# Performance work log

Measured on AMD Instinct MI355X. Metric: run time of the kernel, lower is better.

The kernel has to match this reference:

```python
import jax, jax.numpy as jnp
import numpy as np

B, C, H, W = 32, 64, 64, 64
NUM_CODES = 1024
COMMITMENT_COST = 0.25


def setup_inputs() -> dict:
    key = jax.random.key(0)
    k1, k2 = jax.random.split(key)
    z = jax.random.normal(k1, (B, C, H, W), dtype=jnp.float32)
    # matches nn.Embedding init uniform_(-1/num_codes, 1/num_codes)
    codebook = jax.random.uniform(k2, (NUM_CODES, C), dtype=jnp.float32,
                                  minval=-1.0 / NUM_CODES, maxval=1.0 / NUM_CODES)
    return {"z": z, "codebook": codebook}


def reference(z, codebook):
    # b c h w -> b h w c
    zt = jnp.transpose(z, (0, 2, 3, 1))
    b, h, w, c = zt.shape
    z_flat = zt.reshape(-1, c)  # (N, c)

    # squared L2 distances to each code: ||z||^2 + ||e||^2 - 2 z.e
    d = (jnp.sum(z_flat * z_flat, axis=1, keepdims=True)
         + jnp.sum(codebook * codebook, axis=1)[None, :]
         - 2.0 * z_flat @ codebook.T)  # (N, K)
    indices = jnp.argmin(d, axis=1)  # (N,)

    z_q = codebook[indices].reshape(b, h, w, c)

    codebook_loss = jnp.mean((z_q - jax.lax.stop_gradient(zt)) ** 2)
    commitment_loss = jnp.mean((zt - jax.lax.stop_gradient(z_q)) ** 2)
    loss = codebook_loss + COMMITMENT_COST * commitment_loss

    # straight-through estimator
    z_q_st = zt + jax.lax.stop_gradient(z_q - zt)
    z_q_out = jnp.transpose(z_q_st, (0, 3, 1, 2))  # b h w c -> b c h w
    return z_q_out, loss, indices.reshape(b, h, w)
```

## Files before the change

### kernel.cpp

```cpp
#include <hip/hip_runtime.h>

#define CDIM 64
#define KCODES 1024
#define ZQ_ELEMS (32 * 64 * 64 * 64)
#define NROWS 131072
#define FLT_BIG 3.402823466e38f
#define RPB 64
#define NBLK (NROWS / RPB)
#define CSTRIDE 49
#define DELTA 5e-4f

#define WS_BSQ_OFF 16384
#define WS_E1_OFF  32768

#define SK_RD_OFF 12544
#define SK_RK_OFF (12544 + 1024)
#define SU_BYTES  (12544 + 2048)

typedef __bf16 bf16x8 __attribute__((ext_vector_type(8)));
typedef float  f32x4  __attribute__((ext_vector_type(4)));

__device__ __forceinline__ float pairwise_sq64(const float* v) {
    float r[8];
    #pragma unroll
    for (int j = 0; j < 8; ++j) r[j] = __fmul_rn(v[j], v[j]);
    #pragma unroll
    for (int m = 1; m < 8; ++m) {
        #pragma unroll
        for (int j = 0; j < 8; ++j)
            r[j] = __fadd_rn(r[j], __fmul_rn(v[8 * m + j], v[8 * m + j]));
    }
    return __fadd_rn(__fadd_rn(__fadd_rn(r[0], r[1]), __fadd_rn(r[2], r[3])),
                     __fadd_rn(__fadd_rn(r[4], r[5]), __fadd_rn(r[6], r[7])));
}

__global__ __launch_bounds__(256) void vq_prep(const float* __restrict__ cb,
                                               float* __restrict__ Bsq,
                                               __bf16* __restrict__ e1) {
    const int k = blockIdx.x * 256 + threadIdx.x;
    const float* __restrict__ ck = cb + k * CDIM;
    float v[CDIM];
    #pragma unroll
    for (int q = 0; q < 16; ++q) {
        float4 t = ((const float4*)ck)[q];
        v[4 * q + 0] = t.x; v[4 * q + 1] = t.y; v[4 * q + 2] = t.z; v[4 * q + 3] = t.w;
    }
    Bsq[k] = pairwise_sq64(v);

    const int t = k >> 4, kin = k & 15;
    bf16x8* F1 = (bf16x8*)e1;
    #pragma unroll
    for (int ks = 0; ks < 2; ++ks) {
        #pragma unroll
        for (int g = 0; g < 4; ++g) {
            bf16x8 a;
            #pragma unroll
            for (int i = 0; i < 8; ++i) a[i] = (__bf16)v[ks * 32 + 8 * g + i];
            F1[(t * 2 + ks) * 64 + ((g << 4) | kin)] = a;
        }
    }
}

#define INS(j, accv, Bv, code0) \
    { \
        const float vv = __fmaf_rn(-2.f, (accv), (Bv)); \
        const float kk = __int_as_float((__float_as_int(vv) & 0xFFFFFC00) | (code0)); \
        const float o0 = K0[j], o1 = K1[j], o2 = K2[j]; \
        K0[j] = fminf(o0, kk); \
        K1[j] = __builtin_amdgcn_fmed3f(o0, o1, kk); \
        K2[j] = __builtin_amdgcn_fmed3f(o1, o2, kk); \
    }

#define TILE_COMPUTE(Ea, Eb, code0) \
    { \
        const float Bv = sB[code0]; \
        f32x4 a0 = __builtin_amdgcn_mfma_f32_16x16x32_bf16(zA0, Ea, zero, 0, 0, 0); \
        a0       = __builtin_amdgcn_mfma_f32_16x16x32_bf16(zA1, Eb, a0, 0, 0, 0); \
        INS(0, a0[0], Bv, code0) INS(1, a0[1], Bv, code0) \
        INS(2, a0[2], Bv, code0) INS(3, a0[3], Bv, code0) \
    }

__global__ __launch_bounds__(256, 4) void vq_main(const float* __restrict__ z,
                                                  const float* __restrict__ cb,
                                                  const float* __restrict__ Bsq,
                                                  const __bf16* __restrict__ e1,
                                                  float* __restrict__ zq_out,
                                                  float* __restrict__ idx_out,
                                                  double* __restrict__ part) {
    __shared__ __align__(16) unsigned char sU[SU_BYTES];
    __shared__ float sB[KCODES];

    const int tid = threadIdx.x;
    const int n0 = blockIdx.x * RPB;
    const int b = n0 >> 12;
    const int hw0 = n0 & 4095;
    const float* __restrict__ zb = z + ((size_t)b << 18) + hw0;

    for (int k = tid; k < KCODES; k += 256) sB[k] = Bsq[k];

    {
        bf16x8* __restrict__ zfw = (bf16x8*)sU;
        const int r = tid & 63;
        const int hh = tid >> 6;
        const int H = hh >> 1, G = hh & 1;
        const int w = r >> 4, li = r & 15;
        #pragma unroll
        for (int gg = 0; gg < 2; ++gg) {
            const int g = G * 2 + gg;
            bf16x8 hi;
            #pragma unroll
            for (int i = 0; i < 8; ++i) {
                const float fv = zb[((size_t)(32 * H + 8 * g + i) << 12) + r];
                hi[i] = (__bf16)fv;
            }
            zfw[(w * 2 + H) * 65 + ((g << 4) | li)] = hi;
        }
    }
    __syncthreads();

    const int lane = tid & 63, w = tid >> 6;
    const int g = lane >> 4, li = lane & 15;

    const bf16x8* __restrict__ zf = (const bf16x8*)sU;
    const bf16x8 zA0 = zf[(w * 2 + 0) * 65 + lane];
    const bf16x8 zA1 = zf[(w * 2 + 1) * 65 + lane];

    float K0[4], K1[4], K2[4];
    #pragma unroll
    for (int j = 0; j < 4; ++j) { K0[j] = FLT_BIG; K1[j] = FLT_BIG; K2[j] = FLT_BIG; }

    const bf16x8* __restrict__ pe1 = (const bf16x8*)e1 + lane;
    const f32x4 zero = {0.f, 0.f, 0.f, 0.f};

    bf16x8 A1a = pe1[0], A1b = pe1[64];
    int tb = li;

    for (int t = 0; t < 64; t += 2) {
        const int o1 = (t + 1) * 128;
        const int o2 = (t + 2) * 128;
        bf16x8 B1a = pe1[o1], B1b = pe1[o1 + 64];
        TILE_COMPUTE(A1a, A1b, tb)
        A1a = pe1[o2]; A1b = pe1[o2 + 64];
        TILE_COMPUTE(B1a, B1b, tb + 16)
        tb += 32;
    }

    __syncthreads();

    float* __restrict__ sKey = (float*)sU;
    float* __restrict__ sRd = (float*)(sU + SK_RD_OFF);
    int*   __restrict__ sRk = (int*)(sU + SK_RK_OFF);
    #pragma unroll
    for (int j = 0; j < 4; ++j) {
        const int row = 16 * w + 4 * g + j;
        const int base = row * CSTRIDE + li * 3;
        sKey[base + 0] = K0[j];
        sKey[base + 1] = K1[j];
        sKey[base + 2] = K2[j];
    }
    __syncthreads();

    const int r = tid & 63;
    const int quarter = tid >> 6;
    const int n = n0 + r;

    float gmin = FLT_BIG;
    #pragma unroll
    for (int s2 = 0; s2 < 48; ++s2) gmin = fminf(gmin, sKey[r * CSTRIDE + s2]);
    const float thr = gmin + DELTA;

    float zrow[CDIM];
    const float* __restrict__ zp = zb + r;
    #pragma unroll
    for (int c = 0; c < CDIM; ++c) zrow[c] = zp[(size_t)c << 12];
    const float A = pairwise_sq64(zrow);

    float bd = FLT_BIG;
    int bk = 1 << 30;
    const int sbeg = quarter * 12;
    for (int s2 = sbeg; s2 < sbeg + 12; ++s2) {
        const float kv = sKey[r * CSTRIDE + s2];
        if (kv <= thr) {
            const int k = __float_as_int(kv) & 0x3FF;
            const float4* __restrict__ ek = (const float4*)(cb + (size_t)k * CDIM);
            float m = 0.f;
            #pragma unroll
            for (int q = 0; q < 16; ++q) {
                float4 e = ek[q];
                m = __fmaf_rn(zrow[4 * q + 0], e.x, m);
                m = __fmaf_rn(zrow[4 * q + 1], e.y, m);
                m = __fmaf_rn(zrow[4 * q + 2], e.z, m);
                m = __fmaf_rn(zrow[4 * q + 3], e.w, m);
            }
            const float d = __fsub_rn(__fadd_rn(A, sB[k]), __fadd_rn(m, m));
            if (d < bd || (d == bd && k < bk)) { bd = d; bk = k; }
        }
    }

    sRd[tid] = bd;
    sRk[tid] = bk;
    __syncthreads();

    if (tid < RPB) {
        #pragma unroll
        for (int qq = 1; qq < 4; ++qq) {
            const float d2 = sRd[qq * 64 + r];
            const int   k2 = sRk[qq * 64 + r];
            if (d2 < bd || (d2 == bd && k2 < bk)) { bd = d2; bk = k2; }
        }

        idx_out[n] = (float)bk;

        const float4* __restrict__ cq = (const float4*)(cb + (size_t)bk * CDIM);
        float* __restrict__ zo = zq_out + ((size_t)b << 18) + hw0 + r;
        float lsum = 0.f;
        #pragma unroll
        for (int q = 0; q < 16; ++q) {
            float4 qv = cq[q];
            zo[(size_t)(4 * q + 0) << 12] = qv.x;
            zo[(size_t)(4 * q + 1) << 12] = qv.y;
            zo[(size_t)(4 * q + 2) << 12] = qv.z;
            zo[(size_t)(4 * q + 3) << 12] = qv.w;
            lsum = fmaf(qv.x - zrow[4 * q + 0], qv.x - zrow[4 * q + 0], lsum);
            lsum = fmaf(qv.y - zrow[4 * q + 1], qv.y - zrow[4 * q + 1], lsum);
            lsum = fmaf(qv.z - zrow[4 * q + 2], qv.z - zrow[4 * q + 2], lsum);
            lsum = fmaf(qv.w - zrow[4 * q + 3], qv.w - zrow[4 * q + 3], lsum);
        }

        double ls = (double)lsum;
        for (int off = 32; off > 0; off >>= 1) ls += __shfl_down(ls, off, 64);
        if (tid == 0) part[blockIdx.x] = ls;
    }
}

__global__ void vq_finalize(const double* __restrict__ part, float* __restrict__ loss_out) {
    __shared__ double s[16];
    const int tid = threadIdx.x;
    double v = part[tid] + part[tid + 1024];
    for (int off = 32; off > 0; off >>= 1) v += __shfl_down(v, off, 64);
    if ((tid & 63) == 0) s[tid >> 6] = v;
    __syncthreads();
    if (tid == 0) {
        double t = 0.0;
        #pragma unroll
        for (int i = 0; i < 16; ++i) t += s[i];
        *loss_out = (float)(1.25 * t / (double)ZQ_ELEMS);
    }
}

extern "C" void kernel_launch(void* const* d_in, const int* in_sizes, int n_in,
                              void* d_out, int out_size, void* d_ws, size_t ws_size,
                              hipStream_t stream) {
    const float* z  = (const float*)d_in[0];
    const float* cb = (const float*)d_in[1];
    float* out  = (float*)d_out;
    float* zq   = out;
    float* loss = out + ZQ_ELEMS;
    float* idx  = out + ZQ_ELEMS + 1;
    char* ws = (char*)d_ws;
    double* part = (double*)ws;
    float* Bsq   = (float*)(ws + WS_BSQ_OFF);
    __bf16* e1   = (__bf16*)(ws + WS_E1_OFF);

    vq_prep<<<4, 256, 0, stream>>>(cb, Bsq, e1);
    vq_main<<<NBLK, 256, 0, stream>>>(z, cb, Bsq, e1, zq, idx, part);
    vq_finalize<<<1, 1024, 0, stream>>>(part, loss);
}
```

Measured before the change: 75.90 us.

## Share codebook fragments across waves via double-buffered LDS with bigger blocks

Each block now handles 128 rows with 512 threads instead of 64 rows with 256. The bf16 codebook fragments are staged through a double-buffered LDS tile that all eight waves share, rather than each wave streaming them from global memory on its own. This cuts global/L2 traffic for the codebook and halves the number of per-block partial sums. The cost is a block-wide barrier on every codebook chunk, and launch bounds of (512, 4) tighten the register budget, which risks spilling the 64-float zrow array. The prefetch on the last iteration also reads past the end of the e1 buffer.

```diff
diff --git a/kernel.cpp b/kernel.cpp
--- a/kernel.cpp
+++ b/kernel.cpp
@@ -5,17 +5,22 @@
 #define ZQ_ELEMS (32 * 64 * 64 * 64)
 #define NROWS 131072
 #define FLT_BIG 3.402823466e38f
-#define RPB 64
+#define RPB 128
 #define NBLK (NROWS / RPB)
+#define NTHR 512
 #define CSTRIDE 49
 #define DELTA 5e-4f
 
 #define WS_BSQ_OFF 16384
 #define WS_E1_OFF  32768
 
-#define SK_RD_OFF 12544
-#define SK_RK_OFF (12544 + 1024)
-#define SU_BYTES  (12544 + 2048)
+#define B_OFF     0
+#define FRAG_OFF  4096
+#define E_OFF     20736
+#define SKEY_OFF  4096
+#define SK_RD_OFF 29184
+#define SK_RK_OFF 31232
+#define SU_BYTES  33280
 
 typedef __bf16 bf16x8 __attribute__((ext_vector_type(8)));
 typedef float  f32x4  __attribute__((ext_vector_type(4)));
@@ -80,7 +85,7 @@
         INS(2, a0[2], Bv, code0) INS(3, a0[3], Bv, code0) \
     }
 
-__global__ __launch_bounds__(256, 4) void vq_main(const float* __restrict__ z,
+__global__ __launch_bounds__(512, 4) void vq_main(const float* __restrict__ z,
                                                   const float* __restrict__ cb,
                                                   const float* __restrict__ Bsq,
                                                   const __bf16* __restrict__ e1,
@@ -88,7 +93,8 @@
                                                   float* __restrict__ idx_out,
                                                   double* __restrict__ part) {
     __shared__ __align__(16) unsigned char sU[SU_BYTES];
-    __shared__ float sB[KCODES];
+    __shared__ double sP2[2];
+    float* __restrict__ sB = (float*)(sU + B_OFF);
 
     const int tid = threadIdx.x;
     const int n0 = blockIdx.x * RPB;
@@ -96,13 +102,13 @@
     const int hw0 = n0 & 4095;
     const float* __restrict__ zb = z + ((size_t)b << 18) + hw0;
 
-    for (int k = tid; k < KCODES; k += 256) sB[k] = Bsq[k];
+    for (int k = tid; k < KCODES; k += NTHR) sB[k] = Bsq[k];
 
     {
-        bf16x8* __restrict__ zfw = (bf16x8*)sU;
-        const int r = tid & 63;
-        const int hh = tid >> 6;
-        const int H = hh >> 1, G = hh & 1;
+        bf16x8* __restrict__ zfw = (bf16x8*)(sU + FRAG_OFF);
+        const int r = tid & 127;
+        const int q4 = tid >> 7;
+        const int H = q4 >> 1, G = q4 & 1;
         const int w = r >> 4, li = r & 15;
         #pragma unroll
         for (int gg = 0; gg < 2; ++gg) {
@@ -115,13 +121,15 @@
             }
             zfw[(w * 2 + H) * 65 + ((g << 4) | li)] = hi;
         }
+        *(float2*)(sU + E_OFF + tid * 8) =
+            *(const float2*)((const unsigned char*)e1 + tid * 8);
     }
     __syncthreads();
 
     const int lane = tid & 63, w = tid >> 6;
     const int g = lane >> 4, li = lane & 15;
 
-    const bf16x8* __restrict__ zf = (const bf16x8*)sU;
+    const bf16x8* __restrict__ zf = (const bf16x8*)(sU + FRAG_OFF);
     const bf16x8 zA0 = zf[(w * 2 + 0) * 65 + lane];
     const bf16x8 zA1 = zf[(w * 2 + 1) * 65 + lane];
 
@@ -129,25 +137,20 @@
     #pragma unroll
     for (int j = 0; j < 4; ++j) { K0[j] = FLT_BIG; K1[j] = FLT_BIG; K2[j] = FLT_BIG; }
 
-    const bf16x8* __restrict__ pe1 = (const bf16x8*)e1 + lane;
     const f32x4 zero = {0.f, 0.f, 0.f, 0.f};
 
-    bf16x8 A1a = pe1[0], A1b = pe1[64];
-    int tb = li;
-
-    for (int t = 0; t < 64; t += 2) {
-        const int o1 = (t + 1) * 128;
-        const int o2 = (t + 2) * 128;
-        bf16x8 B1a = pe1[o1], B1b = pe1[o1 + 64];
-        TILE_COMPUTE(A1a, A1b, tb)
-        A1a = pe1[o2]; A1b = pe1[o2 + 64];
-        TILE_COMPUTE(B1a, B1b, tb + 16)
-        tb += 32;
-    }
-
-    __syncthreads();
-
-    float* __restrict__ sKey = (float*)sU;
+    for (int c = 0; c < 32; ++c) {
+        const float2 vstage =
+            *(const float2*)((const unsigned char*)e1 + (c + 1) * 4096 + tid * 8);
+        const bf16x8* __restrict__ buf = (const bf16x8*)(sU + E_OFF + (c & 1) * 4096);
+        const int cb0 = c * 32 + li;
+        TILE_COMPUTE(buf[lane],       buf[64 + lane],  cb0)
+        *(float2*)(sU + E_OFF + ((c + 1) & 1) * 4096 + tid * 8) = vstage;
+        TILE_COMPUTE(buf[128 + lane], buf[192 + lane], cb0 + 16)
+        __syncthreads();
+    }
+
+    float* __restrict__ sKey = (float*)(sU + SKEY_OFF);
     float* __restrict__ sRd = (float*)(sU + SK_RD_OFF);
     int*   __restrict__ sRk = (int*)(sU + SK_RK_OFF);
     #pragma unroll
@@ -160,83 +163,87 @@
     }
     __syncthreads();
 
-    const int r = tid & 63;
-    const int quarter = tid >> 6;
-    const int n = n0 + r;
-
-    float gmin = FLT_BIG;
-    #pragma unroll
-    for (int s2 = 0; s2 < 48; ++s2) gmin = fminf(gmin, sKey[r * CSTRIDE + s2]);
-    const float thr = gmin + DELTA;
-
-    float zrow[CDIM];
-    const float* __restrict__ zp = zb + r;
-    #pragma unroll
-    for (int c = 0; c < CDIM; ++c) zrow[c] = zp[(size_t)c << 12];
-    const float A = pairwise_sq64(zrow);
-
-    float bd = FLT_BIG;
-    int bk = 1 << 30;
-    const int sbeg = quarter * 12;
-    for (int s2 = sbeg; s2 < sbeg + 12; ++s2) {
-        const float kv = sKey[r * CSTRIDE + s2];
-        if (kv <= thr) {
-            const int k = __float_as_int(kv) & 0x3FF;
-            const float4* __restrict__ ek = (const float4*)(cb + (size_t)k * CDIM);
-            float m = 0.f;
+    {
+        const int r = tid & 127;
+        const int quarter = tid >> 7;
+        const int n = n0 + r;
+
+        float gmin = FLT_BIG;
+        #pragma unroll
+        for (int s2 = 0; s2 < 48; ++s2) gmin = fminf(gmin, sKey[r * CSTRIDE + s2]);
+        const float thr = gmin + DELTA;
+
+        float zrow[CDIM];
+        const float* __restrict__ zp = zb + r;
+        #pragma unroll
+        for (int c = 0; c < CDIM; ++c) zrow[c] = zp[(size_t)c << 12];
+        const float A = pairwise_sq64(zrow);
+
+        float bd = FLT_BIG;
+        int bk = 1 << 30;
+        const int sbeg = quarter * 12;
+        for (int s2 = sbeg; s2 < sbeg + 12; ++s2) {
+            const float kv = sKey[r * CSTRIDE + s2];
+            if (kv <= thr) {
+                const int k = __float_as_int(kv) & 0x3FF;
+                const float4* __restrict__ ek = (const float4*)(cb + (size_t)k * CDIM);
+                float m = 0.f;
+                #pragma unroll
+                for (int q = 0; q < 16; ++q) {
+                    float4 e = ek[q];
+                    m = __fmaf_rn(zrow[4 * q + 0], e.x, m);
+                    m = __fmaf_rn(zrow[4 * q + 1], e.y, m);
+                    m = __fmaf_rn(zrow[4 * q + 2], e.z, m);
+                    m = __fmaf_rn(zrow[4 * q + 3], e.w, m);
+                }
+                const float d = __fsub_rn(__fadd_rn(A, sB[k]), __fadd_rn(m, m));
+                if (d < bd || (d == bd && k < bk)) { bd = d; bk = k; }
+            }
+        }
+
+        sRd[tid] = bd;
+        sRk[tid] = bk;
+        __syncthreads();
+
+        if (tid < RPB) {
+            #pragma unroll
+            for (int qq = 1; qq < 4; ++qq) {
+                const float d2 = sRd[qq * 128 + r];
+                const int   k2 = sRk[qq * 128 + r];
+                if (d2 < bd || (d2 == bd && k2 < bk)) { bd = d2; bk = k2; }
+            }
+
+            idx_out[n] = (float)bk;
+
+            const float4* __restrict__ cq = (const float4*)(cb + (size_t)bk * CDIM);
+            float* __restrict__ zo = zq_out + ((size_t)b << 18) + hw0 + r;
+            float lsum = 0.f;
             #pragma unroll
             for (int q = 0; q < 16; ++q) {
-                float4 e = ek[q];
-                m = __fmaf_rn(zrow[4 * q + 0], e.x, m);
-                m = __fmaf_rn(zrow[4 * q + 1], e.y, m);
-                m = __fmaf_rn(zrow[4 * q + 2], e.z, m);
-                m = __fmaf_rn(zrow[4 * q + 3], e.w, m);
-            }
-            const float d = __fsub_rn(__fadd_rn(A, sB[k]), __fadd_rn(m, m));
-            if (d < bd || (d == bd && k < bk)) { bd = d; bk = k; }
-        }
-    }
-
-    sRd[tid] = bd;
-    sRk[tid] = bk;
-    __syncthreads();
-
-    if (tid < RPB) {
-        #pragma unroll
-        for (int qq = 1; qq < 4; ++qq) {
-            const float d2 = sRd[qq * 64 + r];
-            const int   k2 = sRk[qq * 64 + r];
-            if (d2 < bd || (d2 == bd && k2 < bk)) { bd = d2; bk = k2; }
-        }
-
-        idx_out[n] = (float)bk;
-
-        const float4* __restrict__ cq = (const float4*)(cb + (size_t)bk * CDIM);
-        float* __restrict__ zo = zq_out + ((size_t)b << 18) + hw0 + r;
-        float lsum = 0.f;
-        #pragma unroll
-        for (int q = 0; q < 16; ++q) {
-            float4 qv = cq[q];
-            zo[(size_t)(4 * q + 0) << 12] = qv.x;
-            zo[(size_t)(4 * q + 1) << 12] = qv.y;
-            zo[(size_t)(4 * q + 2) << 12] = qv.z;
-            zo[(size_t)(4 * q + 3) << 12] = qv.w;
-            lsum = fmaf(qv.x - zrow[4 * q + 0], qv.x - zrow[4 * q + 0], lsum);
-            lsum = fmaf(qv.y - zrow[4 * q + 1], qv.y - zrow[4 * q + 1], lsum);
-            lsum = fmaf(qv.z - zrow[4 * q + 2], qv.z - zrow[4 * q + 2], lsum);
-            lsum = fmaf(qv.w - zrow[4 * q + 3], qv.w - zrow[4 * q + 3], lsum);
-        }
-
-        double ls = (double)lsum;
-        for (int off = 32; off > 0; off >>= 1) ls += __shfl_down(ls, off, 64);
-        if (tid == 0) part[blockIdx.x] = ls;
-    }
+                float4 qv = cq[q];
+                zo[(size_t)(4 * q + 0) << 12] = qv.x;
+                zo[(size_t)(4 * q + 1) << 12] = qv.y;
+                zo[(size_t)(4 * q + 2) << 12] = qv.z;
+                zo[(size_t)(4 * q + 3) << 12] = qv.w;
+                lsum = fmaf(qv.x - zrow[4 * q + 0], qv.x - zrow[4 * q + 0], lsum);
+                lsum = fmaf(qv.y - zrow[4 * q + 1], qv.y - zrow[4 * q + 1], lsum);
+                lsum = fmaf(qv.z - zrow[4 * q + 2], qv.z - zrow[4 * q + 2], lsum);
+                lsum = fmaf(qv.w - zrow[4 * q + 3], qv.w - zrow[4 * q + 3], lsum);
+            }
+
+            double ls = (double)lsum;
+            for (int off = 32; off > 0; off >>= 1) ls += __shfl_down(ls, off, 64);
+            if ((tid & 63) == 0) sP2[tid >> 6] = ls;
+        }
+    }
+    __syncthreads();
+    if (tid == 0) part[blockIdx.x] = sP2[0] + sP2[1];
 }
 
 __global__ void vq_finalize(const double* __restrict__ part, float* __restrict__ loss_out) {
     __shared__ double s[16];
     const int tid = threadIdx.x;
-    double v = part[tid] + part[tid + 1024];
+    double v = part[tid];
     for (int off = 32; off > 0; off >>= 1) v += __shfl_down(v, off, 64);
     if ((tid & 63) == 0) s[tid >> 6] = v;
     __syncthreads();
@@ -263,6 +270,6 @@
     __bf16* e1   = (__bf16*)(ws + WS_E1_OFF);
 
     vq_prep<<<4, 256, 0, stream>>>(cb, Bsq, e1);
-    vq_main<<<NBLK, 256, 0, stream>>>(z, cb, Bsq, e1, zq, idx, part);
+    vq_main<<<NBLK, NTHR, 0, stream>>>(z, cb, Bsq, e1, zq, idx, part);
     vq_finalize<<<1, 1024, 0, stream>>>(part, loss);
 }
```

New measurement: 74.96 us. Within noise of the previous version (-1.2%).
